# Performance work log

Hardware: AMD Instinct MI355X
Metric: run time of the kernel (lower is better)

## Reference

```python
import jax, jax.numpy as jnp
import numpy as np

B, S, D, H = 2, 2048, 1024, 16
HD = D // H  # head_dim = 64


def setup_inputs() -> dict:
    key = jax.random.key(0)
    ks = jax.random.split(key, 11)
    sc = 1.0 / np.sqrt(D)
    inp = {
        "query": jax.random.normal(ks[0], (B, S, D), jnp.float32),
        "key_": jax.random.normal(ks[1], (B, S, D), jnp.float32),
        "value": jax.random.normal(ks[2], (B, S, D), jnp.float32),
        "Wq": jax.random.normal(ks[3], (D, D), jnp.float32) * sc,
        "bq": jnp.zeros((D,), jnp.float32),
        "Wk": jax.random.normal(ks[4], (D, D), jnp.float32) * sc,
        "bk": jnp.zeros((D,), jnp.float32),
        "Wv": jax.random.normal(ks[5], (D, D), jnp.float32) * sc,
        "bv": jnp.zeros((D,), jnp.float32),
        "Wo": jax.random.normal(ks[6], (D, D), jnp.float32) * sc,
        "bo": jnp.zeros((D,), jnp.float32),
    }
    return inp


def _split_heads(x):
    # [B,S,D] -> [B,H,S,HD]
    return x.reshape(B, -1, H, HD).transpose(0, 2, 1, 3)


def reference(query, key_, value, Wq, bq, Wk, bk, Wv, bv, Wo, bo):
    q = _split_heads(query @ Wq.T + bq)
    k = _split_heads(key_ @ Wk.T + bk)
    v = _split_heads(value @ Wv.T + bv)
    scores = jnp.einsum("bhqd,bhkd->bhqk", q, k) / jnp.sqrt(jnp.float32(HD))
    attn = jax.nn.softmax(scores, axis=-1)  # dropout is identity in eval
    out = jnp.einsum("bhqk,bhkd->bhqd", attn, v)
    out = out.transpose(0, 2, 1, 3).reshape(B, -1, D)
    return out @ Wo.T + bo
```

## Files before the change

kernel.cpp:

```cpp
#include <hip/hip_runtime.h>
#include <hip/hip_bf16.h>
#include <stdint.h>

#define B_  2
#define S_  2048
#define D_  1024
#define H_  16
#define HD_ 64
#define M_  (B_*S_)

typedef __bf16 bf16x8 __attribute__((ext_vector_type(8)));
typedef float  f32x4  __attribute__((ext_vector_type(4)));
typedef unsigned int u32x4 __attribute__((ext_vector_type(4)));
typedef unsigned int u32x2 __attribute__((ext_vector_type(2)));
typedef unsigned short ushort_t;
typedef ushort_t u16x8 __attribute__((ext_vector_type(8)));

#define LOG2E 1.44269504088896f

__device__ __forceinline__ ushort_t f2bf(float f) {
    return __builtin_bit_cast(ushort_t, (__bf16)f);
}
__device__ __forceinline__ bf16x8 load_frag(const ushort_t* p) {
    u32x4 r = *reinterpret_cast<const u32x4*>(p);
    return __builtin_bit_cast(bf16x8, r);
}
__device__ __forceinline__ bf16x8 lds_frag(const ushort_t* p) {
    u32x4 r = *reinterpret_cast<const u32x4*>(p);
    return __builtin_bit_cast(bf16x8, r);
}
__device__ __forceinline__ void gld_lds16(const ushort_t* g, ushort_t* l) {
    __builtin_amdgcn_global_load_lds(
        (const __attribute__((address_space(1))) void*)g,
        (__attribute__((address_space(3))) void*)l, 16, 0, 0);
}

__device__ __forceinline__ void cvt_body(const float* __restrict__ in,
                                         ushort_t* __restrict__ out, int i) {
    f32x4 v0 = *reinterpret_cast<const f32x4*>(in + i);
    f32x4 v1 = *reinterpret_cast<const f32x4*>(in + i + 4);
    u16x8 o;
#pragma unroll
    for (int j = 0; j < 4; ++j) { o[j] = f2bf(v0[j]); o[4 + j] = f2bf(v1[j]); }
    *reinterpret_cast<u16x8*>(out + i) = o;
}

__global__ __launch_bounds__(256) void cvt_all_kernel(
    const float* q, const float* k, const float* v,
    const float* fwq, const float* fwk, const float* fwv, const float* fwo,
    ushort_t* oq, ushort_t* ok, ushort_t* ov,
    ushort_t* owq, ushort_t* owk, ushort_t* owv, ushort_t* owo)
{
    const size_t T = (size_t)M_ * D_;
    const size_t U = (size_t)D_ * D_;
    const size_t idx = ((size_t)blockIdx.x * 256 + threadIdx.x) * 8;
    const float* in; ushort_t* out; size_t off;
    if (idx < 3 * T) {
        const size_t w = idx >> 22; off = idx & (T - 1);
        in  = (w == 0) ? q  : (w == 1) ? k  : v;
        out = (w == 0) ? oq : (w == 1) ? ok : ov;
    } else {
        const size_t r = idx - 3 * T;
        const size_t w = r >> 20; off = r & (U - 1);
        in  = (w == 0) ? fwq : (w == 1) ? fwk : (w == 2) ? fwv : fwo;
        out = (w == 0) ? owq : (w == 1) ? owk : (w == 2) ? owv : owo;
    }
    cvt_body(in, out, (int)off);
}

__device__ __forceinline__ void gemm_body(const ushort_t* __restrict__ X,
                                          const ushort_t* __restrict__ W,
                                          const float* __restrict__ bias,
                                          void* __restrict__ out, int mode)
{
    __shared__ ushort_t lA[128 * 32];
    __shared__ ushort_t lB[128 * 32];

    const int tid  = threadIdx.x;
    const int lane = tid & 63;
    const int wv   = tid >> 6;
    const int m0   = blockIdx.x * 128;
    const int n0   = blockIdx.y * 128;
    const int wr   = (wv >> 1) * 64;
    const int wc   = (wv & 1) * 64;
    const int l15  = lane & 15;
    const int lg   = lane >> 4;

    f32x4 acc[4][4];
#pragma unroll
    for (int i = 0; i < 4; ++i)
#pragma unroll
        for (int j = 0; j < 4; ++j) acc[i][j] = (f32x4){0.f, 0.f, 0.f, 0.f};

    const int srow = lane >> 2;
    const int sk   = (lane & 3) * 8;

    for (int kt = 0; kt < D_ / 32; ++kt) {
        const int k0 = kt * 32;
#pragma unroll
        for (int i = 0; i < 2; ++i) {
            int c = wv * 2 + i;
            gld_lds16(X + (size_t)(m0 + c * 16 + srow) * D_ + k0 + sk, &lA[c * 512]);
        }
#pragma unroll
        for (int i = 0; i < 2; ++i) {
            int c = wv * 2 + i;
            gld_lds16(W + (size_t)(n0 + c * 16 + srow) * D_ + k0 + sk, &lB[c * 512]);
        }
        __syncthreads();

        bf16x8 a[4], b[4];
#pragma unroll
        for (int i = 0; i < 4; ++i)
            a[i] = load_frag(&lA[(wr + i * 16 + l15) * 32 + lg * 8]);
#pragma unroll
        for (int j = 0; j < 4; ++j)
            b[j] = load_frag(&lB[(wc + j * 16 + l15) * 32 + lg * 8]);
#pragma unroll
        for (int i = 0; i < 4; ++i)
#pragma unroll
            for (int j = 0; j < 4; ++j)
                acc[i][j] = __builtin_amdgcn_mfma_f32_16x16x32_bf16(a[i], b[j], acc[i][j], 0, 0, 0);
        __syncthreads();
    }

#pragma unroll
    for (int i = 0; i < 4; ++i) {
#pragma unroll
        for (int j = 0; j < 4; ++j) {
            const int gcol = n0 + wc + j * 16 + l15;
            const float bv = bias[gcol];
#pragma unroll
            for (int r = 0; r < 4; ++r) {
                const int grow = m0 + wr + i * 16 + lg * 4 + r;
                float v = acc[i][j][r] + bv;
                if (mode == 0) v *= 0.125f * LOG2E;
                if (mode == 3) {
                    ((float*)out)[(size_t)grow * D_ + gcol] = v;
                } else {
                    const int b = grow >> 11, s = grow & (S_ - 1);
                    const int h = gcol >> 6,  hd = gcol & 63;
                    size_t addr;
                    if (mode == 2) addr = ((size_t)(b * H_ + h) * HD_ + hd) * S_ + s;
                    else           addr = ((size_t)(b * H_ + h) * S_ + s) * HD_ + hd;
                    ((ushort_t*)out)[addr] = f2bf(v);
                }
            }
        }
    }
}

__global__ __launch_bounds__(256) void qkv_kernel(
    const ushort_t* q_in, const ushort_t* k_in, const ushort_t* v_in,
    const ushort_t* Wq, const ushort_t* Wk, const ushort_t* Wv,
    const float* bq, const float* bk, const float* bv,
    ushort_t* qo, ushort_t* ko, ushort_t* vo)
{
    const int z = blockIdx.z;
    const ushort_t* X  = (z == 0) ? q_in : (z == 1) ? k_in : v_in;
    const ushort_t* W  = (z == 0) ? Wq   : (z == 1) ? Wk   : Wv;
    const float*    bs = (z == 0) ? bq   : (z == 1) ? bk   : bv;
    ushort_t*       o  = (z == 0) ? qo   : (z == 1) ? ko   : vo;
    gemm_body(X, W, bs, o, (z == 2) ? 2 : z);
}

__global__ __launch_bounds__(256) void oproj_kernel(
    const ushort_t* X, const ushort_t* W, const float* bias, float* out)
{
    gemm_body(X, W, bias, out, 3);
}

#define PSTRIDE 72
#define KVB 64
#define NT  (S_ / KVB)
#define AW  8

__global__ __launch_bounds__(512, 4) void attn_kernel(
    const ushort_t* __restrict__ Q, const ushort_t* __restrict__ K,
    const ushort_t* __restrict__ VT, ushort_t* __restrict__ O)
{
    __shared__ ushort_t kbuf[2][KVB * 64];
    __shared__ ushort_t vbuf[2][KVB * 64];
    __shared__ ushort_t plds[AW * 16 * PSTRIDE];

    const int lane  = threadIdx.x & 63;
    const int wv    = threadIdx.x >> 6;
    const int bh    = blockIdx.x;
    const int qb    = blockIdx.y;
    const int qbase = qb * (16 * AW) + wv * 16;
    const int l15   = lane & 15;
    const int lg    = lane >> 4;

    const ushort_t* Qp = Q  + (size_t)bh * S_ * HD_;
    const ushort_t* Kp = K  + (size_t)bh * S_ * HD_;
    const ushort_t* Vp = VT + (size_t)bh * HD_ * S_;

    const int st_id   = threadIdx.x & 255;
    const bool st_k   = (threadIdx.x < 256);
    const ushort_t* Sg = st_k ? Kp : Vp;
    const int gstride  = st_k ? HD_ : S_;
    const int gtile    = st_k ? (KVB * HD_) : KVB;

    const int sm0   = st_id;
    const int srow0 = sm0 >> 3;
    const int scb0  = ((sm0 & 7) ^ (srow0 & 7)) * 8;
    const int sm1   = 256 + st_id;
    const int srow1 = sm1 >> 3;
    const int scb1  = ((sm1 & 7) ^ (srow1 & 7)) * 8;

    int off[4][2];
#pragma unroll
    for (int x = 0; x < 4; ++x)
#pragma unroll
        for (int c = 0; c < 2; ++c)
            off[x][c] = (x * 16 + l15) * 64 + ((c * 32 + lg * 8) ^ ((l15 & 7) << 3));

    bf16x8 aq[2];
#pragma unroll
    for (int c = 0; c < 2; ++c)
        aq[c] = load_frag(Qp + (size_t)(qbase + l15) * HD_ + c * 32 + lg * 8);

    f32x4 accO[4];
#pragma unroll
    for (int dt = 0; dt < 4; ++dt) accO[dt] = (f32x4){0.f, 0.f, 0.f, 0.f};
    float lrun = 0.f;

    ushort_t* pbuf = &plds[wv * 16 * PSTRIDE];

    {
        ushort_t* dst = st_k ? kbuf[0] : vbuf[0];
        gld_lds16(Sg + (size_t)srow0 * gstride + scb0, dst + sm0 * 8);
        gld_lds16(Sg + (size_t)srow1 * gstride + scb1, dst + sm1 * 8);
    }
    __syncthreads();

    for (int t = 0; t < NT; ++t) {
        const int cur = t & 1;
        const ushort_t* kb = kbuf[cur];
        const ushort_t* vb = vbuf[cur];
        if (t + 1 < NT) {
            const ushort_t* g = Sg + (size_t)(t + 1) * gtile;
            ushort_t* dst = st_k ? kbuf[cur ^ 1] : vbuf[cur ^ 1];
            gld_lds16(g + (size_t)srow0 * gstride + scb0, dst + sm0 * 8);
            gld_lds16(g + (size_t)srow1 * gstride + scb1, dst + sm1 * 8);
        }

        f32x4 st[4];
#pragma unroll
        for (int j = 0; j < 4; ++j) st[j] = (f32x4){0.f, 0.f, 0.f, 0.f};
        __builtin_amdgcn_s_setprio(1);
#pragma unroll
        for (int j = 0; j < 4; ++j)
#pragma unroll
            for (int c = 0; c < 2; ++c)
                st[j] = __builtin_amdgcn_mfma_f32_16x16x32_bf16(
                    lds_frag(&kb[off[j][c]]), aq[c], st[j], 0, 0, 0);
        __builtin_amdgcn_s_setprio(0);

        float p[4][4];
#pragma unroll
        for (int j = 0; j < 4; ++j)
#pragma unroll
            for (int r = 0; r < 4; ++r)
                p[j][r] = exp2f(st[j][r]);

#pragma unroll
        for (int j = 0; j < 4; ++j) {
            u32x2 w;
            w[0] = (unsigned)f2bf(p[j][0]) | ((unsigned)f2bf(p[j][1]) << 16);
            w[1] = (unsigned)f2bf(p[j][2]) | ((unsigned)f2bf(p[j][3]) << 16);
            *reinterpret_cast<u32x2*>(&pbuf[l15 * PSTRIDE + j * 16 + lg * 4]) = w;
        }

        float s0 = (p[0][0] + p[0][1]) + (p[0][2] + p[0][3]);
        float s1 = (p[1][0] + p[1][1]) + (p[1][2] + p[1][3]);
        float s2 = (p[2][0] + p[2][1]) + (p[2][2] + p[2][3]);
        float s3 = (p[3][0] + p[3][1]) + (p[3][2] + p[3][3]);
        lrun += (s0 + s1) + (s2 + s3);

        bf16x8 ap[2];
#pragma unroll
        for (int c = 0; c < 2; ++c)
            ap[c] = lds_frag(&pbuf[l15 * PSTRIDE + c * 32 + lg * 8]);

        __builtin_amdgcn_s_setprio(1);
#pragma unroll
        for (int dt = 0; dt < 4; ++dt)
#pragma unroll
            for (int c = 0; c < 2; ++c)
                accO[dt] = __builtin_amdgcn_mfma_f32_16x16x32_bf16(
                    lds_frag(&vb[off[dt][c]]), ap[c], accO[dt], 0, 0, 0);
        __builtin_amdgcn_s_setprio(0);

        __syncthreads();
    }

    lrun += __shfl_xor(lrun, 16);
    lrun += __shfl_xor(lrun, 32);
    const float inv = 1.0f / lrun;
    const int b = bh >> 4, h = bh & 15;
    const size_t rowbase = (size_t)(b * S_ + qbase + l15) * D_ + h * 64;
#pragma unroll
    for (int dt = 0; dt < 4; ++dt) {
        u32x2 w;
        w[0] = (unsigned)f2bf(accO[dt][0] * inv) | ((unsigned)f2bf(accO[dt][1] * inv) << 16);
        w[1] = (unsigned)f2bf(accO[dt][2] * inv) | ((unsigned)f2bf(accO[dt][3] * inv) << 16);
        *reinterpret_cast<u32x2*>(&O[rowbase + dt * 16 + lg * 4]) = w;
    }
}

extern "C" void kernel_launch(void* const* d_in, const int* in_sizes, int n_in,
                              void* d_out, int out_size, void* d_ws, size_t ws_size,
                              hipStream_t stream)
{
    const float* query = (const float*)d_in[0];
    const float* key_  = (const float*)d_in[1];
    const float* value = (const float*)d_in[2];
    const float* Wq    = (const float*)d_in[3];
    const float* bq    = (const float*)d_in[4];
    const float* Wk    = (const float*)d_in[5];
    const float* bk    = (const float*)d_in[6];
    const float* Wv    = (const float*)d_in[7];
    const float* bv    = (const float*)d_in[8];
    const float* Wo    = (const float*)d_in[9];
    const float* bo    = (const float*)d_in[10];

    ushort_t* ws   = (ushort_t*)d_ws;
    const size_t T = (size_t)M_ * D_;
    const size_t U = (size_t)D_ * D_;
    ushort_t* xq  = ws;
    ushort_t* xk  = xq + T;
    ushort_t* xv  = xk + T;
    ushort_t* wq  = xv + T;
    ushort_t* wk  = wq + U;
    ushort_t* wv  = wk + U;
    ushort_t* wo  = wv + U;
    ushort_t* qws  = wo + U;
    ushort_t* kws  = qws + T;
    ushort_t* vtws = kws + T;
    ushort_t* aows = vtws + T;

    const int cvt_blocks = (int)((3 * T + 4 * U) / (256 * 8));
    cvt_all_kernel<<<cvt_blocks, 256, 0, stream>>>(
        query, key_, value, Wq, Wk, Wv, Wo,
        xq, xk, xv, wq, wk, wv, wo);

    qkv_kernel<<<dim3(32, 8, 3), 256, 0, stream>>>(
        xq, xk, xv, wq, wk, wv, bq, bk, bv, qws, kws, vtws);

    attn_kernel<<<dim3(32, 16), 512, 0, stream>>>(qws, kws, vtws, aows);

    oproj_kernel<<<dim3(32, 8, 1), 256, 0, stream>>>(
        aows, wo, bo, (float*)d_out);
}
```

Measured before the change: 140.9 us.

## Double-buffer GEMM LDS tiles and prefetch with explicit vmcnt waits

The projection GEMM gets double-buffered LDS tiles, so the global-to-LDS load for the next K tile is issued before computing on the current one. Both the GEMM and the attention loop replace __syncthreads with raw s_barrier plus explicit vmcnt waits, letting prefetches stay in flight across the barrier. The attention exponent now uses the native exp2 builtin instead of exp2f. The trade-offs are double the GEMM LDS footprint, which may lower occupancy, and hand-placed waitcnt and barriers whose correctness relies on the compiler not reordering LDS accesses around them.

```diff
diff --git a/kernel.cpp b/kernel.cpp
--- a/kernel.cpp
+++ b/kernel.cpp
@@ -17,6 +17,12 @@
 typedef ushort_t u16x8 __attribute__((ext_vector_type(8)));
 
 #define LOG2E 1.44269504088896f
+
+#if __has_builtin(__builtin_amdgcn_exp2f)
+#define EXP2(x) __builtin_amdgcn_exp2f(x)
+#else
+#define EXP2(x) exp2f(x)
+#endif
 
 __device__ __forceinline__ ushort_t f2bf(float f) {
     return __builtin_bit_cast(ushort_t, (__bf16)f);
@@ -73,8 +79,8 @@
                                           const float* __restrict__ bias,
                                           void* __restrict__ out, int mode)
 {
-    __shared__ ushort_t lA[128 * 32];
-    __shared__ ushort_t lB[128 * 32];
+    __shared__ ushort_t lA[2][128 * 32];
+    __shared__ ushort_t lB[2][128 * 32];
 
     const int tid  = threadIdx.x;
     const int lane = tid & 63;
@@ -94,34 +100,45 @@
 
     const int srow = lane >> 2;
     const int sk   = (lane & 3) * 8;
-
-    for (int kt = 0; kt < D_ / 32; ++kt) {
-        const int k0 = kt * 32;
-#pragma unroll
-        for (int i = 0; i < 2; ++i) {
-            int c = wv * 2 + i;
-            gld_lds16(X + (size_t)(m0 + c * 16 + srow) * D_ + k0 + sk, &lA[c * 512]);
+    const int c0   = wv * 2, c1 = wv * 2 + 1;
+    const size_t arow0 = (size_t)(m0 + c0 * 16 + srow) * D_ + sk;
+    const size_t arow1 = (size_t)(m0 + c1 * 16 + srow) * D_ + sk;
+    const size_t brow0 = (size_t)(n0 + c0 * 16 + srow) * D_ + sk;
+    const size_t brow1 = (size_t)(n0 + c1 * 16 + srow) * D_ + sk;
+
+    gld_lds16(X + arow0, &lA[0][c0 * 512]);
+    gld_lds16(X + arow1, &lA[0][c1 * 512]);
+    gld_lds16(W + brow0, &lB[0][c0 * 512]);
+    gld_lds16(W + brow1, &lB[0][c1 * 512]);
+
+    const int NKT = D_ / 32;
+    for (int kt = 0; kt < NKT; ++kt) {
+        const int cur = kt & 1;
+        __builtin_amdgcn_s_barrier();
+        if (kt + 1 < NKT) {
+            const int k0 = (kt + 1) * 32;
+            gld_lds16(X + arow0 + k0, &lA[cur ^ 1][c0 * 512]);
+            gld_lds16(X + arow1 + k0, &lA[cur ^ 1][c1 * 512]);
+            gld_lds16(W + brow0 + k0, &lB[cur ^ 1][c0 * 512]);
+            gld_lds16(W + brow1 + k0, &lB[cur ^ 1][c1 * 512]);
+            asm volatile("s_waitcnt vmcnt(4)" ::: "memory");
+        } else {
+            asm volatile("s_waitcnt vmcnt(0)" ::: "memory");
         }
-#pragma unroll
-        for (int i = 0; i < 2; ++i) {
-            int c = wv * 2 + i;
-            gld_lds16(W + (size_t)(n0 + c * 16 + srow) * D_ + k0 + sk, &lB[c * 512]);
-        }
-        __syncthreads();
+        __builtin_amdgcn_s_barrier();
 
         bf16x8 a[4], b[4];
 #pragma unroll
         for (int i = 0; i < 4; ++i)
-            a[i] = load_frag(&lA[(wr + i * 16 + l15) * 32 + lg * 8]);
+            a[i] = lds_frag(&lA[cur][(wr + i * 16 + l15) * 32 + lg * 8]);
 #pragma unroll
         for (int j = 0; j < 4; ++j)
-            b[j] = load_frag(&lB[(wc + j * 16 + l15) * 32 + lg * 8]);
+            b[j] = lds_frag(&lB[cur][(wc + j * 16 + l15) * 32 + lg * 8]);
 #pragma unroll
         for (int i = 0; i < 4; ++i)
 #pragma unroll
             for (int j = 0; j < 4; ++j)
                 acc[i][j] = __builtin_amdgcn_mfma_f32_16x16x32_bf16(a[i], b[j], acc[i][j], 0, 0, 0);
-        __syncthreads();
     }
 
 #pragma unroll
@@ -232,18 +249,23 @@
         gld_lds16(Sg + (size_t)srow0 * gstride + scb0, dst + sm0 * 8);
         gld_lds16(Sg + (size_t)srow1 * gstride + scb1, dst + sm1 * 8);
     }
-    __syncthreads();
 
     for (int t = 0; t < NT; ++t) {
         const int cur = t & 1;
         const ushort_t* kb = kbuf[cur];
         const ushort_t* vb = vbuf[cur];
+
+        __builtin_amdgcn_s_barrier();
         if (t + 1 < NT) {
             const ushort_t* g = Sg + (size_t)(t + 1) * gtile;
             ushort_t* dst = st_k ? kbuf[cur ^ 1] : vbuf[cur ^ 1];
             gld_lds16(g + (size_t)srow0 * gstride + scb0, dst + sm0 * 8);
             gld_lds16(g + (size_t)srow1 * gstride + scb1, dst + sm1 * 8);
+            asm volatile("s_waitcnt vmcnt(2)" ::: "memory");
+        } else {
+            asm volatile("s_waitcnt vmcnt(0)" ::: "memory");
         }
+        __builtin_amdgcn_s_barrier();
 
         f32x4 st[4];
 #pragma unroll
@@ -262,7 +284,7 @@
         for (int j = 0; j < 4; ++j)
 #pragma unroll
             for (int r = 0; r < 4; ++r)
-                p[j][r] = exp2f(st[j][r]);
+                p[j][r] = EXP2(st[j][r]);
 
 #pragma unroll
         for (int j = 0; j < 4; ++j) {
@@ -291,8 +313,6 @@
                 accO[dt] = __builtin_amdgcn_mfma_f32_16x16x32_bf16(
                     lds_frag(&vb[off[dt][c]]), ap[c], accO[dt], 0, 0, 0);
         __builtin_amdgcn_s_setprio(0);
-
-        __syncthreads();
     }
 
     lrun += __shfl_xor(lrun, 16);
```

Measured after the change: 137.1 us. 1.03x faster.
